# Kernel tuning notes

Measured on AMD Instinct MI355X. Metric: run time of the kernel, lower is better.

## Reference

```python
import jax, jax.numpy as jnp
import numpy as np

EPS = float(np.finfo(np.float32).eps)
B, N, NUM_ATOM, K = 16, 256, 64, 20
NUM_EDGETYPE = 3
SHORT = (1, 2, 3)
LONG = (3, 5, 7)
HIDDEN = (128, 128)
OUT = 1
SCALES = len(SHORT) + len(LONG) + NUM_EDGETYPE + 1  # 10
LB = 1e-4  # lanczos breakdown tolerance


def _xavier(k, fi, fo):
    return jax.random.uniform(k, (fi, fo), jnp.float32, -1.0, 1.0) * (6.0 / (fi + fo)) ** 0.5


def setup_inputs() -> dict:
    key = jax.random.key(0)
    ks = jax.random.split(key, 12)
    inp = {}
    inp["node_feat"] = jax.random.randint(ks[0], (B, N), 0, NUM_ATOM)
    inp["L"] = jax.random.uniform(ks[1], (B, N, N, NUM_EDGETYPE + 1), jnp.float32)
    # embedding_map: Linear(num_atom,1024) -> ReLU -> Linear(1024,num_atom)
    inp["emb_w1"] = _xavier(ks[2], NUM_ATOM, 1024); inp["emb_b1"] = jnp.zeros((1024,), jnp.float32)
    inp["emb_w2"] = _xavier(ks[3], 1024, NUM_ATOM); inp["emb_b2"] = jnp.zeros((NUM_ATOM,), jnp.float32)
    # eigen_map per long scale: Linear(K*K,1024) -> ReLU -> Linear(1024,K*K)
    S, K2 = len(LONG), K * K
    inp["eig_w1"] = jnp.stack([_xavier(jax.random.fold_in(ks[4], i), K2, 1024) for i in range(S)])
    inp["eig_b1"] = jnp.zeros((S, 1024), jnp.float32)
    inp["eig_w2"] = jnp.stack([_xavier(jax.random.fold_in(ks[5], i), 1024, K2) for i in range(S)])
    inp["eig_b2"] = jnp.zeros((S, K2), jnp.float32)
    dims = [NUM_ATOM] + list(HIDDEN) + [OUT]
    inp["filt_w0"] = _xavier(ks[6], dims[0] * SCALES, dims[1]); inp["filt_b0"] = jnp.zeros((dims[1],), jnp.float32)
    inp["filt_w1"] = _xavier(ks[7], dims[1] * SCALES, dims[2]); inp["filt_b1"] = jnp.zeros((dims[2],), jnp.float32)
    inp["filt_wo"] = _xavier(ks[8], dims[2], dims[3]); inp["filt_bo"] = jnp.zeros((dims[3],), jnp.float32)
    inp["att_w"] = _xavier(ks[9], dims[2], 1); inp["att_b"] = jnp.zeros((1,), jnp.float32)
    return inp


def _graph_laplacian(feat, adj_mask):
    # feat: B x N x D; pairwise gaussian affinity, sym-normalized (alpha=0.5)
    diff = feat[:, :, None, :] - feat[:, None, :, :]           # B,N,N,D
    dist2 = jnp.sum(diff * diff, axis=-1).reshape(B, -1)       # B,N*N
    sigma2 = jnp.mean(dist2, axis=1, keepdims=True)
    A = jnp.exp(-dist2 / sigma2).reshape(B, N, N) * adj_mask
    row_sum = jnp.sum(A, axis=2, keepdims=True)
    pad = jnp.where(row_sum == 0.0, 1.0, 0.0)
    D = 1.0 / jnp.sqrt(row_sum + pad)
    return D * A * jnp.swapaxes(D, 1, 2)


def _lanczos(A, key):
    # sequential Lanczos tridiagonalization with double Gram-Schmidt reorth
    q = jax.random.normal(key, (B, N), jnp.float32)
    q = q / jnp.linalg.norm(q, axis=1, keepdims=True)

    def step(carry, i):
        Qbuf, q_prev, qc, beta_prev, valid = carry
        z = jnp.einsum('bij,bj->bi', A, qc)
        alpha = jnp.sum(qc * z, axis=1)
        z = z - alpha[:, None] * qc - beta_prev[:, None] * q_prev
        for _ in range(2):  # reorthogonalize against Q[1..ii-1] (zero cols are no-ops)
            coef = jnp.einsum('bnk,bn->bk', Qbuf, z) / (jnp.sum(Qbuf * Qbuf, axis=1) + EPS)
            z = z - jnp.einsum('bnk,bk->bn', Qbuf, coef)
        beta = jnp.sqrt(jnp.sum(z * z, axis=1))
        valid = valid * (beta >= LB).astype(jnp.float32)
        q_next = z * valid[:, None] / (beta[:, None] + EPS)
        Qbuf = Qbuf.at[:, :, i].set(qc)
        return (Qbuf, qc, q_next, beta, valid), (alpha, beta, valid, qc)

    init = (jnp.zeros((B, N, K), jnp.float32), jnp.zeros((B, N), jnp.float32), q,
            jnp.zeros((B,), jnp.float32), jnp.ones((B,), jnp.float32))
    _, (alphas, betas, valids, qs) = jax.lax.scan(step, init, jnp.arange(K))
    alpha = alphas.T            # B,K
    beta = betas.T              # B,K
    valid = valids.T            # B,K (cumulative 1..1 0..0)
    idx = jnp.sum(valid, axis=1).astype(jnp.int32)   # rank per sample
    alpha = alpha * valid
    beta = beta[:, :K - 1] * valid[:, :K - 1]
    T = jax.vmap(lambda a, b: jnp.diag(a) + jnp.diag(b, 1) + jnp.diag(b, -1))(alpha, beta)
    Q = jnp.transpose(qs, (1, 2, 0))  # B,N,K
    # faithful to source: zero node rows >= idx_mask (only when idx < N)
    row_ok = (jnp.arange(N)[None, :] < idx[:, None]) | (idx[:, None] >= N)
    Q = Q * valid[:, None, :] * row_ok[:, :, None].astype(jnp.float32)
    return T, Q


def _spectral_filters(T, Q, eig_w1, eig_b1, eig_w2, eig_b2, key):
    T_list = []
    TT = T
    b = jax.random.normal(key, (B, K, 1), jnp.float32)
    Tb = b / jnp.linalg.norm(b, axis=1, keepdims=True)
    for ii in range(max(LONG) + 1):
        if ii in LONG:
            T_list.append(TT)
        TT = TT @ T
        # power-iteration cap on spectral radius
        Tb_new = T @ Tb
        l_max = jnp.sum(Tb_new * Tb, axis=1, keepdims=True) / (jnp.sum(Tb * Tb, axis=1, keepdims=True) + EPS)
        TT = TT * (jnp.abs(l_max) <= 1.0).astype(jnp.float32)
        Tb = Tb_new / (jnp.linalg.norm(Tb_new, axis=1, keepdims=True) + EPS)
    triu = jnp.triu(jnp.ones((K, K), jnp.float32))
    eye = jnp.eye(K, dtype=jnp.float32)
    outs = []
    for s in range(len(LONG)):
        h = jax.nn.relu(T_list[s].reshape(B, -1) @ eig_w1[s] + eig_b1[s])
        DD = (h @ eig_w2[s] + eig_b2[s]).reshape(B, K, K)
        DD = DD * triu
        DD = DD + jnp.swapaxes(DD, 1, 2) * (1.0 - eye)  # symmetrize
        outs.append(jnp.einsum('bnk,bkl,bml->bnm', Q, DD, Q))
    return jnp.stack(outs, axis=3)  # B,N,N,S


def reference(node_feat, L, emb_w1, emb_b1, emb_w2, emb_b2, eig_w1, eig_b1, eig_w2, eig_b2,
              filt_w0, filt_b0, filt_w1, filt_b1, filt_wo, filt_bo, att_w, att_b):
    key = jax.random.key(42)
    state = jax.nn.one_hot(node_feat, NUM_ATOM, dtype=jnp.float32)  # frozen identity embedding
    feat = jax.nn.relu(state @ emb_w1 + emb_b1) @ emb_w2 + emb_b2
    Lk = _graph_laplacian(feat, L[:, :, :, 0])
    T, Q = _lanczos(Lk, jax.random.fold_in(key, 0))
    filt_w = (filt_w0, filt_w1)
    filt_b = (filt_b0, filt_b1)
    for tt in range(len(HIDDEN)):
        msg = []
        DD = _spectral_filters(T, Q, eig_w1, eig_b1, eig_w2, eig_b2, jax.random.fold_in(key, tt + 1))
        tmp = state
        for ii in range(1, max(SHORT) + 1):  # short diffusion
            tmp = jnp.einsum('bij,bjd->bid', Lk, tmp)
            if ii in SHORT:
                msg.append(tmp)
        for s in range(len(LONG)):           # long (spectral) diffusion
            msg.append(jnp.einsum('bij,bjd->bid', DD[:, :, :, s], state))
        for e in range(NUM_EDGETYPE + 1):     # per-edgetype propagation
            msg.append(jnp.einsum('bij,bjd->bid', L[:, :, :, e], state))
        msg = jnp.concatenate(msg, axis=2)    # B,N,10*D
        state = jax.nn.relu(msg @ filt_w[tt] + filt_b[tt])
    y = state @ filt_wo + filt_bo             # B,N,1
    att = jax.nn.sigmoid(state @ att_w + att_b)
    score = jnp.mean(att * y, axis=1)          # B,OUT (mask=None -> mean over nodes)
    return score
```

## Files before the change

### kernel.cpp

```cpp
#include <hip/hip_runtime.h>


constexpr int nB = 16;
constexpr int nN = 256;
constexpr int nK = 20;
constexpr int QS = nN + 1;
constexpr float EPSF = 1.1920928955078125e-07f;
constexpr float LBF  = 1e-4f;

#define DEV static __device__ __forceinline__

DEV void tf2x32(unsigned k0, unsigned k1, unsigned x0, unsigned x1,
                unsigned &o0, unsigned &o1) {
  unsigned ks2 = k0 ^ k1 ^ 0x1BD11BDAu;
#define RND(r) { x0 += x1; x1 = (x1 << r) | (x1 >> (32 - r)); x1 ^= x0; }
  x0 += k0;  x1 += k1;
  RND(13) RND(15) RND(26) RND(6)
  x0 += k1;  x1 += ks2 + 1u;
  RND(17) RND(29) RND(16) RND(24)
  x0 += ks2; x1 += k0 + 2u;
  RND(13) RND(15) RND(26) RND(6)
  x0 += k0;  x1 += k1 + 3u;
  RND(17) RND(29) RND(16) RND(24)
  x0 += k1;  x1 += ks2 + 4u;
  RND(13) RND(15) RND(26) RND(6)
  x0 += ks2; x1 += k0 + 5u;
#undef RND
  o0 = x0; o1 = x1;
}

DEV float erfinv_f32(float x) {
  float w = -log1pf(-x * x);
  float p;
  if (w < 5.0f) {
    w -= 2.5f;
    p = 2.81022636e-08f;
    p = fmaf(p, w, 3.43273939e-07f);
    p = fmaf(p, w, -3.5233877e-06f);
    p = fmaf(p, w, -4.39150654e-06f);
    p = fmaf(p, w, 0.00021858087f);
    p = fmaf(p, w, -0.00125372503f);
    p = fmaf(p, w, -0.00417768164f);
    p = fmaf(p, w, 0.246640727f);
    p = fmaf(p, w, 1.50140941f);
  } else {
    w = sqrtf(w) - 3.0f;
    p = -0.000200214257f;
    p = fmaf(p, w, 0.000100950558f);
    p = fmaf(p, w, 0.00134934322f);
    p = fmaf(p, w, -0.00367342844f);
    p = fmaf(p, w, 0.00573950773f);
    p = fmaf(p, w, -0.0076224613f);
    p = fmaf(p, w, 0.00943887047f);
    p = fmaf(p, w, 1.00167406f);
    p = fmaf(p, w, 2.83297682f);
  }
  return p * x;
}

DEV float jax_normal(unsigned k0, unsigned k1, unsigned idx) {
  unsigned o0, o1;
  tf2x32(k0, k1, 0u , idx , o0, o1);
  unsigned bits = o0 ^ o1;
  float u = __uint_as_float((bits >> 9) | 0x3f800000u) - 1.0f;
  const float lo = -0.99999994f;
  float v = fmaxf(lo, u * 2.0f + lo);
  return 1.41421356237309515f * erfinv_f32(v);
}

DEV double waveRedD(double v) {
#pragma unroll
  for (int m = 32; m > 0; m >>= 1) v += __shfl_xor(v, m, 64);
  return v;
}
DEV float waveRedF(float v) {
#pragma unroll
  for (int m = 32; m > 0; m >>= 1) v += __shfl_xor(v, m, 64);
  return v;
}
DEV double blockSumD(double v, double *s4) {
  v = waveRedD(v);
  int w = threadIdx.x >> 6;
  __syncthreads();
  if ((threadIdx.x & 63) == 0) s4[w] = v;
  __syncthreads();
  return s4[0] + s4[1] + s4[2] + s4[3];
}
DEV double sum8(const double *r) {
  return ((r[0] + r[1]) + (r[2] + r[3])) + ((r[4] + r[5]) + (r[6] + r[7]));
}

__global__ __launch_bounds__(256) void feat_table_kernel(
    const float *__restrict__ w1, const float *__restrict__ b1,
    const float *__restrict__ w2, const float *__restrict__ b2,
    float *__restrict__ table) {
  int a = blockIdx.x, t = threadIdx.x;
  __shared__ float hh[1024];
  __shared__ float part[256];
  for (int k = t; k < 1024; k += 256)
    hh[k] = fmaxf(w1[(size_t)a * 1024 + k] + b1[k], 0.f);
  __syncthreads();
  int d = t & 63, slice = t >> 6;
  float acc = 0.f;
  for (int k = slice * 256; k < slice * 256 + 256; k++)
    acc += hh[k] * w2[(size_t)k * 64 + d];
  part[t] = acc;
  __syncthreads();
  if (t < 64)
    table[(size_t)a * 64 + t] =
        part[t] + part[64 + t] + part[128 + t] + part[192 + t] + b2[t];
}

__global__ __launch_bounds__(256) void feat_state_tr_kernel(
    const int *__restrict__ nf, const float *__restrict__ table,
    float *__restrict__ feat, float *__restrict__ featT,
    float *__restrict__ state0) {
  int g = blockIdx.x;
  int bb = g >> 2, n0 = (g & 3) * 64;
  int t = threadIdx.x;
  int c = t & 63, r4 = t >> 6;
  __shared__ float tl[64][65];
  __shared__ int av[64];
  if (t < 64) av[t] = nf[bb * nN + n0 + t];
  __syncthreads();
  for (int r = r4; r < 64; r += 4) {
    int a = av[r];
    float v = table[(size_t)a * 64 + c];
    tl[r][c] = v;
    feat[((size_t)(bb * nN + n0 + r)) * 64 + c] = v;
    state0[((size_t)(bb * nN + n0 + r)) * 64 + c] = (c == a) ? 1.f : 0.f;
  }
  __syncthreads();
  for (int r = r4; r < 64; r += 4)
    featT[(size_t)bb * 16384 + (size_t)r * nN + n0 + c] = tl[c][r];
}

__global__ __launch_bounds__(256) void dist2_kernel(
    const float *__restrict__ feat, const float *__restrict__ featT,
    float *__restrict__ G, double *__restrict__ part) {
  int g = blockIdx.x;
  int bb = g >> 6, i0 = (g & 63) * 4;
  int t = threadIdx.x;
  __shared__ float fi[4][64];
  __shared__ double s4[4];
  {
// ... 201 lines not shown
      Qb[i * QS + t] = qc[t];
      if (t == 0) qn2[i] = (float)sum8(redB);
    }
    __syncthreads();
    if (gid < i) {
      double p = 0.0;
#pragma unroll
      for (int j = 0; j < 16; j++) {
        int n0 = gl + 16 * j;
        p += (double)Qb[gid * QS + n0] * (double)zz[n0];
      }
#pragma unroll
      for (int m = 1; m <= 8; m <<= 1) p += __shfl_xor(p, m, 64);
      if (gl == 0)
        coef[gid] = (float)(p / ((double)qn2[gid] + (double)EPSF));
    }
    __syncthreads();
    if (h == 0) {
      double sub = 0.0;
      for (int k = 0; k < i; k++)
        sub += (double)Qb[k * QS + t] * (double)coef[k];
      zz[t] = (float)((double)zz[t] - sub);
    }
    __syncthreads();
    if (gid < i) {
      double p = 0.0;
#pragma unroll
      for (int j = 0; j < 16; j++) {
        int n0 = gl + 16 * j;
        p += (double)Qb[gid * QS + n0] * (double)zz[n0];
      }
#pragma unroll
      for (int m = 1; m <= 8; m <<= 1) p += __shfl_xor(p, m, 64);
      if (gl == 0)
        coef[gid] = (float)(p / ((double)qn2[gid] + (double)EPSF));
    }
    __syncthreads();
    double bpart = 0.0;
    if (h == 0) {
      double sub = 0.0;
      for (int k = 0; k < i; k++)
        sub += (double)Qb[k * QS + t] * (double)coef[k];
      float znew = (float)((double)zz[t] - sub);
      zz[t] = znew;
      bpart = (double)znew * (double)znew;
    }
    bpart = waveRedD(bpart);
    if (lane == 0) redA[wv] = bpart;
    __syncthreads();
    float beta = sqrtf((float)sum8(redA));
    validf *= (beta >= LBF) ? 1.f : 0.f;
    if (u == 0) {
      sAl[i] = alpha;
      sBe[i] = beta;
      sVa[i] = validf;
    }
    if (h == 0) {
      float qnext = zz[t] * validf / (beta + EPSF);
      qp[t] = qc[t];
      qc[t] = qnext;
    }
    __syncthreads();
    beta_prev = beta;
  }

  float idxf = 0.f;
  for (int k = 0; k < nK; k++) idxf += sVa[k];
  int idx = (int)idxf;
  if (h == 0) {
    float rowok = ((t < idx) || (idx >= nN)) ? 1.f : 0.f;
    for (int k = 0; k < nK; k++)
      Qout[((size_t)bb * nN + t) * nK + k] = Qb[k * QS + t] * sVa[k] * rowok;
  }
  for (int e = u; e < nK * nK; e += 512) {
    int i = e / nK, j = e % nK;
    float v = 0.f;
    if (i == j) v = sAl[i] * sVa[i];
    else if (j == i + 1) v = sBe[i] * sVa[i];
    else if (i == j + 1) v = sBe[j] * sVa[j];
    Tout[(size_t)bb * nK * nK + e] = v;
  }
}

DEV void spect_body(const float *__restrict__ Tin, float *__restrict__ Tpow2,
                    int bb, int tt, int t, char *smem) {
  float *T_  = (float *)smem;
  float *TT  = T_ + nK * nK;
  float *TTn = TT + nK * nK;
  float *Tb  = TTn + nK * nK;
  float *Tbn = Tb + nK;
  for (int e = t; e < nK * nK; e += 64) {
    float v = Tin[(size_t)bb * nK * nK + e];
    T_[e] = v;
    TT[e] = v;
  }
  unsigned k0, k1;
  tf2x32(0u, 42u, 0u, (unsigned)(tt + 1), k0, k1);
  if (t < nK) Tb[t] = jax_normal(k0, k1, (unsigned)(bb * nK + t));
  __syncthreads();
  float pv = (t < nK) ? Tb[t] * Tb[t] : 0.f;
  float nb = sqrtf(waveRedF(pv));
  if (t < nK) Tb[t] = Tb[t] / nb;
  __syncthreads();
  for (int ii = 0; ii < 8; ii++) {
    if (ii == 3 || ii == 5 || ii == 7) {
      int s = (ii - 3) / 2;
      int sf = tt * 3 + s;
      for (int e = t; e < nK * nK; e += 64)
        Tpow2[((size_t)sf * nB + bb) * nK * nK + e] = TT[e];
    }
    __syncthreads();
    for (int e = t; e < nK * nK; e += 64) {
      int i = e / nK, j = e % nK;
      float a = 0.f;
      for (int l = 0; l < nK; l++) a += TT[i * nK + l] * T_[l * nK + j];
      TTn[e] = a;
    }
    if (t < nK) {
      float a = 0.f;
      for (int l = 0; l < nK; l++) a += T_[t * nK + l] * Tb[l];
      Tbn[t] = a;
    }
    __syncthreads();
    float pn = (t < nK) ? Tbn[t] * Tb[t] : 0.f;
    float pd = (t < nK) ? Tb[t] * Tb[t] : 0.f;
    float num = waveRedF(pn);
    float den = waveRedF(pd);
    float lmax = num / (den + EPSF);
    float keep = (fabsf(lmax) <= 1.0f) ? 1.f : 0.f;
    __syncthreads();
    for (int e = t; e < nK * nK; e += 64) TT[e] = TTn[e] * keep;
    float p2 = (t < nK) ? Tbn[t] * Tbn[t] : 0.f;
    float nn = sqrtf(waveRedF(p2));
    if (t < nK) Tb[t] = Tbn[t] / (nn + EPSF);
    __syncthreads();
  }
}

DEV void eig1_body(const float *__restrict__ Tpow2, const float *__restrict__ w1p,
                   const float *__restrict__ b1p, float *__restrict__ h2,
                   int g, int t, char *smem) {
  int oc = g & 15, sf = g >> 4;
  int sw = sf % 3;
  int o = (t & 63) + oc * 64, bbg = t >> 6;
  float *tp = (float *)smem;
  for (int e = t; e < nB * 400; e += 256)
    tp[e] = Tpow2[(size_t)sf * nB * 400 + e];
  __syncthreads();
  float bias = b1p[(size_t)sw * 1024 + o];
  float acc0 = bias, acc1 = bias, acc2 = bias, acc3 = bias;
  const float *W = w1p + (size_t)sw * 400 * 1024 + o;
  const float *t0 = tp + (bbg + 0) * 400;
  const float *t1 = tp + (bbg + 4) * 400;
  const float *t2 = tp + (bbg + 8) * 400;
  const float *t3 = tp + (bbg + 12) * 400;
  for (int k = 0; k < 400; k++) {
    float w = W[(size_t)k * 1024];
    acc0 += t0[k] * w;
    acc1 += t1[k] * w;
    acc2 += t2[k] * w;
    acc3 += t3[k] * w;
  }
  h2[((size_t)sf * nB + (bbg + 0))  * 1024 + o] = fmaxf(acc0, 0.f);
  h2[((size_t)sf * nB + (bbg + 4))  * 1024 + o] = fmaxf(acc1, 0.f);
  h2[((size_t)sf * nB + (bbg + 8))  * 1024 + o] = fmaxf(acc2, 0.f);
  h2[((size_t)sf * nB + (bbg + 12)) * 1024 + o] = fmaxf(acc3, 0.f);
}

DEV void eig2_body(const float *__restrict__ h2, const float *__restrict__ w2p,
                   const float *__restrict__ b2p, float *__restrict__ raw2,
                   int g, int t, char *smem) {
  int kc = g % 25, sf = g / 25;
  int sw = sf % 3;
  int kl = (t & 15) + kc * 16, bb = t >> 4;
  float *hh = (float *)smem;
  for (int e = t; e < nB * 1024; e += 256)
    hh[(e >> 10) * 1025 + (e & 1023)] = h2[(size_t)sf * nB * 1024 + e];
  __syncthreads();
  float acc = b2p[(size_t)sw * 400 + kl];
  const float *W = w2p + (size_t)sw * 1024 * 400 + kl;
  const float *hv = hh + bb * 1025;
  for (int o = 0; o < 1024; o++) acc += hv[o] * W[(size_t)o * 400];
  raw2[((size_t)sf * nB + bb) * 400 + kl] = acc;
}

DEV void qtstate_body(const float *__restrict__ Q, const float *__restrict__ state,
                      float *__restrict__ E, int g, int t, int Din, char *smem) {
  int k = g % nK, bb = g / nK;
  float *qcol = (float *)smem;
  for (int n = t; n < nN; n += Din)
    qcol[n] = Q[((size_t)bb * nN + n) * nK + k];
  __syncthreads();
  const float *st = state + (size_t)bb * nN * Din;
  float acc = 0.f;
  for (int n = 0; n < nN; n++) acc += qcol[n] * st[(size_t)n * Din + t];
  E[((size_t)bb * nK + k) * Din + t] = acc;
}

DEV void lk_body(const float *__restrict__ Lk, const float *__restrict__ in,
                 int inStride, float *__restrict__ out, int outStride,
                 int g, int t, int Din, char *smem) {
  int bb = g >> 5, r0 = (g & 31) * 8;
  float (*rows)[nN] = (float (*)[nN])smem;
  for (int e = t; e < 8 * nN; e += Din) {
    int r = e >> 8, j = e & 255;
    rows[r][j] = Lk[((size_t)bb * nN + r0 + r) * nN + j];
  }
  __syncthreads();
  float acc[8] = {0.f, 0.f, 0.f, 0.f, 0.f, 0.f, 0.f, 0.f};
  const float *ip = in + (size_t)bb * nN * inStride + t;
  for (int j = 0; j < nN; j++) {
    float x = ip[(size_t)j * inStride];
#pragma unroll
    for (int r = 0; r < 8; r++) acc[r] += rows[r][j] * x;
  }
#pragma unroll
  for (int r = 0; r < 8; r++)
    out[((size_t)bb * nN + r0 + r) * outStride + t] = acc[r];
}

DEV void edgemsg_body(const float *__restrict__ Lfull,
                      const float *__restrict__ state, float *__restrict__ msg,
                      int C, int g, int t, int Din, char *smem) {
  int bb = g >> 6, r0 = (g & 63) * 4;
  float4 (*rows4)[nN] = (float4 (*)[nN])smem;
  const float4 *L4 = (const float4 *)Lfull;
  for (int e = t; e < 4 * nN; e += Din) {
    int r = e >> 8, j = e & 255;
    rows4[r][j] = L4[((size_t)bb * nN + r0 + r) * nN + j];
  }
  __syncthreads();
  float acc[4][4];
#pragma unroll
  for (int r = 0; r < 4; r++)
#pragma unroll
    for (int e = 0; e < 4; e++) acc[r][e] = 0.f;
  const float *st = state + (size_t)bb * nN * Din + t;
  for (int j = 0; j < nN; j++) {
    float x = st[(size_t)j * Din];
#pragma unroll
    for (int r = 0; r < 4; r++) {
      float4 lv = rows4[r][j];
      acc[r][0] += lv.x * x;
      acc[r][1] += lv.y * x;
      acc[r][2] += lv.z * x;
      acc[r][3] += lv.w * x;
    }
  }
#pragma unroll
  for (int r = 0; r < 4; r++)
#pragma unroll
    for (int e = 0; e < 4; e++)
      msg[((size_t)bb * nN + r0 + r) * C + (6 + e) * Din + t] = acc[r][e];
}

DEV void ddE_body(const float *__restrict__ raw, const float *__restrict__ E,
                  float *__restrict__ F, int g, int t, int Din, char *smem) {
  int k = g % nK, bb = (g / nK) % nB, s = g / (nK * nB);
  float *dr = (float *)smem;
  if (t < nK) {
    int mi = k < t ? k : t, ma = k < t ? t : k;
    dr[t] = raw[((size_t)s * nB + bb) * 400 + mi * nK + ma];
  }
  __syncthreads();
  float acc = 0.f;
  for (int l = 0; l < nK; l++)
    acc += dr[l] * E[((size_t)bb * nK + l) * Din + t];
  F[(((size_t)s * nB + bb) * nK + k) * Din + t] = acc;
}

DEV void longmsg_body(const float *__restrict__ Q, const float *__restrict__ F,
                      float *__restrict__ msg, int C, int g, int t, int Din,
                      char *smem) {
  int i = g % nN, bb = g / nN;
  float *qr = (float *)smem;
  if (t < nK) qr[t] = Q[((size_t)bb * nN + i) * nK + t];
  __syncthreads();
  for (int s = 0; s < 3; s++) {
    float acc = 0.f;
    for (int k = 0; k < nK; k++)
      acc += qr[k] * F[(((size_t)s * nB + bb) * nK + k) * Din + t];
    msg[((size_t)bb * nN + i) * C + (3 + s) * Din + t] = acc;
  }
}

__global__ __launch_bounds__(64) void l1d1_spect_kernel(
    const float *__restrict__ T, float *__restrict__ Tpow2) {
  __shared__ __align__(16) char smem[5120];
  int bb = blockIdx.x & 15, tt = blockIdx.x >> 4;
  spect_body(T, Tpow2, bb, tt, threadIdx.x, smem);
}

__global__ __launch_bounds__(256) void l1d2_kernel(
    const float *__restrict__ Tpow2, const float *__restrict__ w1p,
    const float *__restrict__ b1p, float *__restrict__ h2,
    const float *__restrict__ Q, const float *__restrict__ state0,
    float *__restrict__ E, const float *__restrict__ Lk,
    float *__restrict__ msg, int C) {
  __shared__ __align__(16) char smem[26240];
  int t = threadIdx.x;
  int gb = blockIdx.x;
  if (gb < 96) {
    eig1_body(Tpow2, w1p, b1p, h2, gb, t, smem);
  } else if (gb < 96 + 320) {
    int g = gb - 96;
    int k = g % nK, bb = g / nK;
    float *qcol = (float *)smem;
    for (int n = t; n < nN; n += 256)
      qcol[n] = Q[((size_t)bb * nN + n) * nK + k];
    __syncthreads();
    if (t < 64) {
      const float *st = state0 + (size_t)bb * nN * 64;
      float acc = 0.f;
      for (int n = 0; n < nN; n++) acc += qcol[n] * st[(size_t)n * 64 + t];
      E[((size_t)bb * nK + k) * 64 + t] = acc;
    }
  } else {
    int g = gb - 416;
    int bb = g >> 5, r0 = (g & 31) * 8;
    float (*rows)[nN] = (float (*)[nN])smem;
    for (int e = t; e < 8 * nN; e += 256) {
      int r = e >> 8, j = e & 255;
      rows[r][j] = Lk[((size_t)bb * nN + r0 + r) * nN + j];
    }
    __syncthreads();
    if (t < 64) {
      float acc[8] = {0.f, 0.f, 0.f, 0.f, 0.f, 0.f, 0.f, 0.f};
      const float *ip = msg + (size_t)bb * nN * C + 0 * 64 + t;
      for (int j = 0; j < nN; j++) {
        float x = ip[(size_t)j * C];
#pragma unroll
        for (int r = 0; r < 8; r++) acc[r] += rows[r][j] * x;
      }
#pragma unroll
      for (int r = 0; r < 8; r++)
        msg[((size_t)bb * nN + r0 + r) * C + 1 * 64 + t] = acc[r];
    }
  }
}

__global__ __launch_bounds__(256) void l1d3_kernel(
    const float *__restrict__ h2, const float *__restrict__ w2p,
    const float *__restrict__ b2p, float *__restrict__ raw2,
    const float *__restrict__ Lk, float *__restrict__ msg, int C) {
  __shared__ __align__(16) char smem[65600];
  int t = threadIdx.x;
  int gb = blockIdx.x;
  if (gb < 150) {
    eig2_body(h2, w2p, b2p, raw2, gb, t, smem);
  } else {
    int g = gb - 150;
    int bb = g >> 5, r0 = (g & 31) * 8;
    float (*rows)[nN] = (float (*)[nN])smem;
    for (int e = t; e < 8 * nN; e += 256) {
      int r = e >> 8, j = e & 255;
      rows[r][j] = Lk[((size_t)bb * nN + r0 + r) * nN + j];
    }
    __syncthreads();
    if (t < 64) {
      float acc[8] = {0.f, 0.f, 0.f, 0.f, 0.f, 0.f, 0.f, 0.f};
      const float *ip = msg + (size_t)bb * nN * C + 1 * 64 + t;
      for (int j = 0; j < nN; j++) {
        float x = ip[(size_t)j * C];
#pragma unroll
        for (int r = 0; r < 8; r++) acc[r] += rows[r][j] * x;
      }
#pragma unroll
      for (int r = 0; r < 8; r++)
        msg[((size_t)bb * nN + r0 + r) * C + 2 * 64 + t] = acc[r];
    }
  }
}

__global__ void msgD1_kernel(const float *__restrict__ Q,
                             const float *__restrict__ state,
                             float *__restrict__ E,
                             const float *__restrict__ Lk,
                             float *__restrict__ msg,
                             const float *__restrict__ Lfull, int C) {
  __shared__ __align__(16) char smem[16384];
  int t = threadIdx.x, Din = blockDim.x;
  int gb = blockIdx.x;
  if (gb < nB * nK) {
    qtstate_body(Q, state, E, gb, t, Din, smem);
  } else if (gb < nB * nK + nB * nN / 8) {
    lk_body(Lk, state, Din, msg + 0 * Din, C, gb - nB * nK, t, Din, smem);
  } else {
    edgemsg_body(Lfull, state, msg, C, gb - nB * nK - nB * nN / 8, t, Din, smem);
  }
}

__global__ void msgD2_kernel(const float *__restrict__ raw,
                             const float *__restrict__ E,
                             float *__restrict__ F,
                             const float *__restrict__ Lk,
                             float *__restrict__ msg, int C, int withLk) {
  __shared__ __align__(16) char smem[8192];
  int t = threadIdx.x, Din = blockDim.x;
  int gb = blockIdx.x;
  if (gb < 3 * nB * nK) {
    ddE_body(raw, E, F, gb, t, Din, smem);
  } else {
    lk_body(Lk, msg + 0 * Din, C, msg + 1 * Din, C, gb - 3 * nB * nK, t, Din,
            smem);
  }
}

__global__ void msgD3_kernel(const float *__restrict__ Q,
                             const float *__restrict__ F,
                             const float *__restrict__ Lk,
                             float *__restrict__ msg, int C) {
  __shared__ __align__(16) char smem[8192];
  int t = threadIdx.x, Din = blockDim.x;
  int gb = blockIdx.x;
  if (gb < nB * nN) {
    longmsg_body(Q, F, msg, C, gb, t, Din, smem);
  } else {
    lk_body(Lk, msg + 1 * Din, C, msg + 2 * Din, C, gb - nB * nN, t, Din, smem);
  }
}

__global__ __launch_bounds__(256) void filt_kernel(
    const float *__restrict__ msg, const float *__restrict__ W,
    const float *__restrict__ bias, float *__restrict__ out, int C) {
  int g = blockIdx.x;
  int base = g * 16;
  int t = threadIdx.x;
  int o = t & 127, ih = t >> 7;
  __shared__ float mt[16][64];
  __shared__ float wt[64][128];
  float acc[8];
  float bo = bias[o];
#pragma unroll
  for (int r = 0; r < 8; r++) acc[r] = bo;
  for (int c0 = 0; c0 < C; c0 += 64) {
    __syncthreads();
    for (int e = t; e < 16 * 64; e += 256) {
      int r = e >> 6, c = e & 63;
      mt[r][c] = msg[((size_t)(base + r)) * C + c0 + c];
    }
    for (int e = t; e < 64 * 128; e += 256)
      wt[e >> 7][e & 127] = W[(size_t)(c0 + (e >> 7)) * 128 + (e & 127)];
    __syncthreads();
    for (int c = 0; c < 64; c++) {
      float w = wt[c][o];
#pragma unroll
      for (int r = 0; r < 8; r++) acc[r] += mt[ih * 8 + r][c] * w;
    }
  }
#pragma unroll
  for (int r = 0; r < 8; r++)
    out[((size_t)(base + ih * 8 + r)) * 128 + o] = fmaxf(acc[r], 0.f);
}

__global__ __launch_bounds__(256) void score_kernel(
    const float *__restrict__ state, const float *__restrict__ wo,
    const float *__restrict__ bo, const float *__restrict__ aw,
    const float *__restrict__ ab, float *__restrict__ out) {
  __shared__ float sl[64 * 129];
  __shared__ double s4[4];
  int bb = blockIdx.x, t = threadIdx.x;
  float bof = bo[0], abf = ab[0];
  double dsum = 0.0;
  for (int r0 = 0; r0 < nN; r0 += 64) {
    __syncthreads();
    for (int e = t; e < 64 * 128; e += 256) {
      int r = e >> 7, o = e & 127;
      sl[r * 129 + o] = state[((size_t)bb * nN + r0 + r) * 128 + o];
    }
    __syncthreads();
    if (t < 64) {
      const float *sr = sl + t * 129;
      float sy = bof, sa = abf;
      for (int o = 0; o < 128; o++) {
        float v = sr[o];
        sy += v * wo[o];
        sa += v * aw[o];
      }
      float att = 1.f / (1.f + expf(-sa));
      dsum += (double)(att * sy);
    }
  }
  double m = blockSumD(dsum, s4);
  if (t == 0) out[bb] = (float)(m / (double)nN);
}

extern "C" void kernel_launch(void *const *d_in, const int *in_sizes, int n_in,
                              void *d_out, int out_size, void *d_ws,
                              size_t ws_size, hipStream_t stream) {
  (void)in_sizes; (void)n_in; (void)out_size;
  const int   *node_feat = (const int *)d_in[0];
  const float *Lfull     = (const float *)d_in[1];
  const float *emb_w1    = (const float *)d_in[2];
  const float *emb_b1    = (const float *)d_in[3];
  const float *emb_w2    = (const float *)d_in[4];
  const float *emb_b2    = (const float *)d_in[5];
  const float *eig_w1    = (const float *)d_in[6];
  const float *eig_b1    = (const float *)d_in[7];
  const float *eig_w2    = (const float *)d_in[8];
  const float *eig_b2    = (const float *)d_in[9];
  const float *filt_w0   = (const float *)d_in[10];
  const float *filt_b0   = (const float *)d_in[11];
  const float *filt_w1   = (const float *)d_in[12];
  const float *filt_b1   = (const float *)d_in[13];
  const float *filt_wo   = (const float *)d_in[14];
  const float *filt_bo   = (const float *)d_in[15];
  const float *att_w     = (const float *)d_in[16];
  const float *att_b     = (const float *)d_in[17];

  float *ws   = (float *)d_ws;
  float *G    = ws;
  float *msg  = G + 1048576;
  float *st0  = msg + 5242880;
  float *st1  = st0 + 262144;
  float *st2  = st1 + 524288;
  float *feat = st2 + 524288;
  float *table= feat + 262144;
  float *Q    = table + 4096;
  float *T    = Q + 81920;
  float *Tpow = T + 6400;
  float *DD   = Tpow + 19200;
  float *h    = DD + 19200;
  float *E    = h + 49152;
  float *F    = E + 40960;
  float *Dv   = F + 122880;
  double *part   = (double *)(Dv + 4096);
  float *GT    = msg + 4194304;
  float *featT = msg + 1048576;
  float *Tpow2 = feat;
  float *raw2  = feat + 38400;
  float *h2    = feat + 76800;
  const size_t needBytes = (size_t)(8220432) * 4;
  if (ws_size < needBytes) return;

  feat_table_kernel<<<64, 256, 0, stream>>>(emb_w1, emb_b1, emb_w2, emb_b2, table);
  feat_state_tr_kernel<<<nB * 4, 256, 0, stream>>>(node_feat, table, feat,
                                                   featT, st0);
  dist2_kernel<<<nB * 64, 256, 0, stream>>>(feat, featT, G, part);
  arow_kernel<<<nB * nN, 256, 0, stream>>>(Lfull, part, G, Dv);
  lkscale_tr_kernel<<<nB * 16, 256, 0, stream>>>(G, Dv, GT);
  lanczos_kernel<<<16 + 512 + 1024, 512, 0, stream>>>(GT, Q, T, st0, Lfull, G,
                                                      msg);

  const int QTB = nB * nK;
  const int LKB = nB * nN / 8;
  const int EDB = nB * nN / 4;
  const int DDB = 3 * nB * nK;
  const int LMB = nB * nN;

  {
    int Din = 64, C = 640;
    const float *rawT = raw2;
    l1d1_spect_kernel<<<nB * 2, 64, 0, stream>>>(T, Tpow2);
    l1d2_kernel<<<96 + QTB + LKB, 256, 0, stream>>>(Tpow2, eig_w1, eig_b1, h2,
                                                    Q, st0, E, G, msg, C);
    l1d3_kernel<<<150 + LKB, 256, 0, stream>>>(h2, eig_w2, eig_b2, raw2, G,
                                               msg, C);
    msgD2_kernel<<<DDB, Din, 0, stream>>>(rawT, E, F, G, msg, C, 0);
    msgD3_kernel<<<LMB, Din, 0, stream>>>(Q, F, G, msg, C);
    filt_kernel<<<nB * nN / 16, 256, 0, stream>>>(msg, filt_w0, filt_b0, st1, C);
  }
  {
    int Din = 128, C = 1280;
    const float *rawT = raw2 + (size_t)3 * nB * 400;
    msgD1_kernel<<<QTB + LKB + EDB, Din, 0, stream>>>(Q, st1, E, G, msg,
                                                      Lfull, C);
    msgD2_kernel<<<DDB + LKB, Din, 0, stream>>>(rawT, E, F, G, msg, C, 1);
    msgD3_kernel<<<LMB + LKB, Din, 0, stream>>>(Q, F, G, msg, C);
    filt_kernel<<<nB * nN / 16, 256, 0, stream>>>(msg, filt_w1, filt_b1, st2, C);
  }
  score_kernel<<<nB, 256, 0, stream>>>(st2, filt_wo, filt_bo, att_w, att_b,
                                       (float *)d_out);
}
```

Baseline: 602.5 us.

## Fuse post-Lanczos stages into persistent megakernel with global atomic barriers

```diff
diff --git a/kernel.cpp b/kernel.cpp
--- a/kernel.cpp
+++ b/kernel.cpp
@@ -60,7 +60,7 @@
 
 DEV float jax_normal(unsigned k0, unsigned k1, unsigned idx) {
   unsigned o0, o1;
-  tf2x32(k0, k1, 0u , idx , o0, o1);
+  tf2x32(k0, k1, 0u, idx, o0, o1);
   unsigned bits = o0 ^ o1;
   float u = __uint_as_float((bits >> 9) | 0x3f800000u) - 1.0f;
   const float lo = -0.99999994f;
@@ -428,35 +428,49 @@
   }
 }
 
-DEV void spect_body(const float *__restrict__ Tin, float *__restrict__ Tpow2,
-                    int bb, int tt, int t, char *smem) {
-  float *T_  = (float *)smem;
-  float *TT  = T_ + nK * nK;
-  float *TTn = TT + nK * nK;
-  float *Tb  = TTn + nK * nK;
+DEV void gbar(unsigned *ctr, int idx, unsigned expect) {
+  __syncthreads();
+  if (threadIdx.x == 0) {
+    __threadfence();
+    atomicAdd(&ctr[idx], 1u);
+    while (atomicAdd(&ctr[idx], 0u) < expect) __builtin_amdgcn_s_sleep(2);
+    __threadfence();
+  }
+  __syncthreads();
+}
+
+DEV void spect256(const float *Tin, float *Tpow2, int bb, int tt, int t,
+                  char *smemc, float *sKeep) {
+  float *T_  = (float *)smemc;
+  float *TT  = T_ + 400;
+  float *TTn = TT + 400;
+  float *Tb  = TTn + 400;
   float *Tbn = Tb + nK;
-  for (int e = t; e < nK * nK; e += 64) {
-    float v = Tin[(size_t)bb * nK * nK + e];
+  for (int e = t; e < 400; e += 256) {
+    float v = Tin[(size_t)bb * 400 + e];
     T_[e] = v;
     TT[e] = v;
   }
-  unsigned k0, k1;
-  tf2x32(0u, 42u, 0u, (unsigned)(tt + 1), k0, k1);
-  if (t < nK) Tb[t] = jax_normal(k0, k1, (unsigned)(bb * nK + t));
-  __syncthreads();
-  float pv = (t < nK) ? Tb[t] * Tb[t] : 0.f;
-  float nb = sqrtf(waveRedF(pv));
-  if (t < nK) Tb[t] = Tb[t] / nb;
+  if (t < nK) {
+    unsigned k0, k1;
+    tf2x32(0u, 42u, 0u, (unsigned)(tt + 1), k0, k1);
+    Tb[t] = jax_normal(k0, k1, (unsigned)(bb * nK + t));
+  }
+  __syncthreads();
+  if (t < 64) {
+    float pv = (t < nK) ? Tb[t] * Tb[t] : 0.f;
+    float nb = sqrtf(waveRedF(pv));
+    if (t < nK) Tb[t] = Tb[t] / nb;
+  }
   __syncthreads();
   for (int ii = 0; ii < 8; ii++) {
     if (ii == 3 || ii == 5 || ii == 7) {
-      int s = (ii - 3) / 2;
-      int sf = tt * 3 + s;
-      for (int e = t; e < nK * nK; e += 64)
-        Tpow2[((size_t)sf * nB + bb) * nK * nK + e] = TT[e];
-    }
-    __syncthreads();
-    for (int e = t; e < nK * nK; e += 64) {
+      int sf = tt * 3 + (ii - 3) / 2;
+      for (int e = t; e < 400; e += 256)
+        Tpow2[((size_t)sf * nB + bb) * 400 + e] = TT[e];
+    }
+    __syncthreads();
+    for (int e = t; e < 400; e += 256) {
       int i = e / nK, j = e % nK;
       float a = 0.f;
       for (int l = 0; l < nK; l++) a += TT[i * nK + l] * T_[l * nK + j];
@@ -468,28 +482,33 @@
       Tbn[t] = a;
     }
     __syncthreads();
-    float pn = (t < nK) ? Tbn[t] * Tb[t] : 0.f;
-    float pd = (t < nK) ? Tb[t] * Tb[t] : 0.f;
-    float num = waveRedF(pn);
-    float den = waveRedF(pd);
-    float lmax = num / (den + EPSF);
-    float keep = (fabsf(lmax) <= 1.0f) ? 1.f : 0.f;
-    __syncthreads();
-    for (int e = t; e < nK * nK; e += 64) TT[e] = TTn[e] * keep;
-    float p2 = (t < nK) ? Tbn[t] * Tbn[t] : 0.f;
-    float nn = sqrtf(waveRedF(p2));
-    if (t < nK) Tb[t] = Tbn[t] / (nn + EPSF);
-    __syncthreads();
-  }
-}
-
-DEV void eig1_body(const float *__restrict__ Tpow2, const float *__restrict__ w1p,
-                   const float *__restrict__ b1p, float *__restrict__ h2,
-                   int g, int t, char *smem) {
+    if (t < 64) {
+      float pn = (t < nK) ? Tbn[t] * Tb[t] : 0.f;
+      float pd = (t < nK) ? Tb[t] * Tb[t] : 0.f;
+      float num = waveRedF(pn);
+      float den = waveRedF(pd);
+      float lmax = num / (den + EPSF);
+      if (t == 0) *sKeep = (fabsf(lmax) <= 1.0f) ? 1.f : 0.f;
+    }
+    __syncthreads();
+    float keep = *sKeep;
+    for (int e = t; e < 400; e += 256) TT[e] = TTn[e] * keep;
+    if (t < 64) {
+      float p2 = (t < nK) ? Tbn[t] * Tbn[t] : 0.f;
+      float nn = sqrtf(waveRedF(p2));
+      if (t < nK) Tb[t] = Tbn[t] / (nn + EPSF);
+    }
+    __syncthreads();
+  }
+  __syncthreads();
+}
+
+DEV void eig1_256(const float *Tpow2, const float *w1p, const float *b1p,
+                  float *h2, int g, int t, char *smemc) {
   int oc = g & 15, sf = g >> 4;
   int sw = sf % 3;
   int o = (t & 63) + oc * 64, bbg = t >> 6;
-  float *tp = (float *)smem;
+  float *tp = (float *)smemc;
   for (int e = t; e < nB * 400; e += 256)
     tp[e] = Tpow2[(size_t)sf * nB * 400 + e];
   __syncthreads();
@@ -511,15 +530,15 @@
   h2[((size_t)sf * nB + (bbg + 4))  * 1024 + o] = fmaxf(acc1, 0.f);
   h2[((size_t)sf * nB + (bbg + 8))  * 1024 + o] = fmaxf(acc2, 0.f);
   h2[((size_t)sf * nB + (bbg + 12)) * 1024 + o] = fmaxf(acc3, 0.f);
-}
-
-DEV void eig2_body(const float *__restrict__ h2, const float *__restrict__ w2p,
-                   const float *__restrict__ b2p, float *__restrict__ raw2,
-                   int g, int t, char *smem) {
+  __syncthreads();
+}
+
+DEV void eig2_256(const float *h2, const float *w2p, const float *b2p,
+                  float *raw2, int g, int t, char *smemc) {
   int kc = g % 25, sf = g / 25;
   int sw = sf % 3;
   int kl = (t & 15) + kc * 16, bb = t >> 4;
-  float *hh = (float *)smem;
+  float *hh = (float *)smemc;
   for (int e = t; e < nB * 1024; e += 256)
     hh[(e >> 10) * 1025 + (e & 1023)] = h2[(size_t)sf * nB * 1024 + e];
   __syncthreads();
@@ -528,253 +547,127 @@
   const float *hv = hh + bb * 1025;
   for (int o = 0; o < 1024; o++) acc += hv[o] * W[(size_t)o * 400];
   raw2[((size_t)sf * nB + bb) * 400 + kl] = acc;
-}
-
-DEV void qtstate_body(const float *__restrict__ Q, const float *__restrict__ state,
-                      float *__restrict__ E, int g, int t, int Din, char *smem) {
+  __syncthreads();
+}
+
+DEV void qt256(const float *Q, const float *state, float *E, int g, int t,
+               int Din, char *smemc) {
   int k = g % nK, bb = g / nK;
-  float *qcol = (float *)smem;
-  for (int n = t; n < nN; n += Din)
+  float *qcol = (float *)smemc;
+  for (int n = t; n < nN; n += 256)
     qcol[n] = Q[((size_t)bb * nN + n) * nK + k];
   __syncthreads();
-  const float *st = state + (size_t)bb * nN * Din;
-  float acc = 0.f;
-  for (int n = 0; n < nN; n++) acc += qcol[n] * st[(size_t)n * Din + t];
-  E[((size_t)bb * nK + k) * Din + t] = acc;
-}
-
-DEV void lk_body(const float *__restrict__ Lk, const float *__restrict__ in,
-                 int inStride, float *__restrict__ out, int outStride,
-                 int g, int t, int Din, char *smem) {
+  if (t < Din) {
+    const float *st = state + (size_t)bb * nN * Din;
+    float acc = 0.f;
+    for (int n = 0; n < nN; n++) acc += qcol[n] * st[(size_t)n * Din + t];
+    E[((size_t)bb * nK + k) * Din + t] = acc;
+  }
+  __syncthreads();
+}
+
+DEV void lk256(const float *Lk, const float *in, int inStride, float *out,
+               int outStride, int g, int t, int Din, char *smemc) {
   int bb = g >> 5, r0 = (g & 31) * 8;
-  float (*rows)[nN] = (float (*)[nN])smem;
-  for (int e = t; e < 8 * nN; e += Din) {
+  float (*rows)[nN] = (float (*)[nN])smemc;
+  for (int e = t; e < 8 * nN; e += 256) {
     int r = e >> 8, j = e & 255;
     rows[r][j] = Lk[((size_t)bb * nN + r0 + r) * nN + j];
   }
   __syncthreads();
-  float acc[8] = {0.f, 0.f, 0.f, 0.f, 0.f, 0.f, 0.f, 0.f};
-  const float *ip = in + (size_t)bb * nN * inStride + t;
-  for (int j = 0; j < nN; j++) {
-    float x = ip[(size_t)j * inStride];
-#pragma unroll
-    for (int r = 0; r < 8; r++) acc[r] += rows[r][j] * x;
-  }
-#pragma unroll
-  for (int r = 0; r < 8; r++)
-    out[((size_t)bb * nN + r0 + r) * outStride + t] = acc[r];
-}
-
-DEV void edgemsg_body(const float *__restrict__ Lfull,
-                      const float *__restrict__ state, float *__restrict__ msg,
-                      int C, int g, int t, int Din, char *smem) {
+  if (t < Din) {
+    float acc[8] = {0.f, 0.f, 0.f, 0.f, 0.f, 0.f, 0.f, 0.f};
+    const float *ip = in + (size_t)bb * nN * inStride + t;
+    for (int j = 0; j < nN; j++) {
+      float x = ip[(size_t)j * inStride];
+#pragma unroll
+      for (int r = 0; r < 8; r++) acc[r] += rows[r][j] * x;
+    }
+#pragma unroll
+    for (int r = 0; r < 8; r++)
+      out[((size_t)bb * nN + r0 + r) * outStride + t] = acc[r];
+  }
+  __syncthreads();
+}
+
+DEV void edge256(const float *Lfull, const float *state, float *msg, int C,
+                 int g, int t, int Din, char *smemc) {
   int bb = g >> 6, r0 = (g & 63) * 4;
-  float4 (*rows4)[nN] = (float4 (*)[nN])smem;
+  float4 (*rows4)[nN] = (float4 (*)[nN])smemc;
   const float4 *L4 = (const float4 *)Lfull;
-  for (int e = t; e < 4 * nN; e += Din) {
+  for (int e = t; e < 4 * nN; e += 256) {
     int r = e >> 8, j = e & 255;
     rows4[r][j] = L4[((size_t)bb * nN + r0 + r) * nN + j];
   }
   __syncthreads();
-  float acc[4][4];
-#pragma unroll
-  for (int r = 0; r < 4; r++)
-#pragma unroll
-    for (int e = 0; e < 4; e++) acc[r][e] = 0.f;
-  const float *st = state + (size_t)bb * nN * Din + t;
-  for (int j = 0; j < nN; j++) {
-    float x = st[(size_t)j * Din];
-#pragma unroll
-    for (int r = 0; r < 4; r++) {
-      float4 lv = rows4[r][j];
-      acc[r][0] += lv.x * x;
-      acc[r][1] += lv.y * x;
-      acc[r][2] += lv.z * x;
-      acc[r][3] += lv.w * x;
-    }
-  }
-#pragma unroll
-  for (int r = 0; r < 4; r++)
-#pragma unroll
-    for (int e = 0; e < 4; e++)
-      msg[((size_t)bb * nN + r0 + r) * C + (6 + e) * Din + t] = acc[r][e];
-}
-
-DEV void ddE_body(const float *__restrict__ raw, const float *__restrict__ E,
-                  float *__restrict__ F, int g, int t, int Din, char *smem) {
+  if (t < Din) {
+    float acc[4][4];
+#pragma unroll
+    for (int r = 0; r < 4; r++)
+#pragma unroll
+      for (int e = 0; e < 4; e++) acc[r][e] = 0.f;
+    const float *st = state + (size_t)bb * nN * Din + t;
+    for (int j = 0; j < nN; j++) {
+      float x = st[(size_t)j * Din];
+#pragma unroll
+      for (int r = 0; r < 4; r++) {
+        float4 lv = rows4[r][j];
+        acc[r][0] += lv.x * x;
+        acc[r][1] += lv.y * x;
+        acc[r][2] += lv.z * x;
+        acc[r][3] += lv.w * x;
+      }
+    }
+#pragma unroll
+    for (int r = 0; r < 4; r++)
+#pragma unroll
+      for (int e = 0; e < 4; e++)
+        msg[((size_t)bb * nN + r0 + r) * C + (6 + e) * Din + t] = acc[r][e];
+  }
+  __syncthreads();
+}
+
+DEV void ddE256(const float *raw, const float *E, float *F, int g, int t,
+                int Din, char *smemc) {
   int k = g % nK, bb = (g / nK) % nB, s = g / (nK * nB);
-  float *dr = (float *)smem;
+  float *dr = (float *)smemc;
   if (t < nK) {
     int mi = k < t ? k : t, ma = k < t ? t : k;
     dr[t] = raw[((size_t)s * nB + bb) * 400 + mi * nK + ma];
   }
   __syncthreads();
-  float acc = 0.f;
-  for (int l = 0; l < nK; l++)
-    acc += dr[l] * E[((size_t)bb * nK + l) * Din + t];
-  F[(((size_t)s * nB + bb) * nK + k) * Din + t] = acc;
-}
-
-DEV void longmsg_body(const float *__restrict__ Q, const float *__restrict__ F,
-                      float *__restrict__ msg, int C, int g, int t, int Din,
-                      char *smem) {
+  if (t < Din) {
+    float acc = 0.f;
+    for (int l = 0; l < nK; l++)
+      acc += dr[l] * E[((size_t)bb * nK + l) * Din + t];
+    F[(((size_t)s * nB + bb) * nK + k) * Din + t] = acc;
+  }
+  __syncthreads();
+}
+
+DEV void longmsg256(const float *Q, const float *F, float *msg, int C, int g,
+                    int t, int Din, char *smemc) {
   int i = g % nN, bb = g / nN;
-  float *qr = (float *)smem;
+  float *qr = (float *)smemc;
   if (t < nK) qr[t] = Q[((size_t)bb * nN + i) * nK + t];
   __syncthreads();
-  for (int s = 0; s < 3; s++) {
-    float acc = 0.f;
-    for (int k = 0; k < nK; k++)
-      acc += qr[k] * F[(((size_t)s * nB + bb) * nK + k) * Din + t];
-    msg[((size_t)bb * nN + i) * C + (3 + s) * Din + t] = acc;
-  }
-}
-
-__global__ __launch_bounds__(64) void l1d1_spect_kernel(
-    const float *__restrict__ T, float *__restrict__ Tpow2) {
-  __shared__ __align__(16) char smem[5120];
-  int bb = blockIdx.x & 15, tt = blockIdx.x >> 4;
-  spect_body(T, Tpow2, bb, tt, threadIdx.x, smem);
-}
-
-__global__ __launch_bounds__(256) void l1d2_kernel(
-    const float *__restrict__ Tpow2, const float *__restrict__ w1p,
-    const float *__restrict__ b1p, float *__restrict__ h2,
-    const float *__restrict__ Q, const float *__restrict__ state0,
-    float *__restrict__ E, const float *__restrict__ Lk,
-    float *__restrict__ msg, int C) {
-  __shared__ __align__(16) char smem[26240];
-  int t = threadIdx.x;
-  int gb = blockIdx.x;
-  if (gb < 96) {
-    eig1_body(Tpow2, w1p, b1p, h2, gb, t, smem);
-  } else if (gb < 96 + 320) {
-    int g = gb - 96;
-    int k = g % nK, bb = g / nK;
-    float *qcol = (float *)smem;
-    for (int n = t; n < nN; n += 256)
-      qcol[n] = Q[((size_t)bb * nN + n) * nK + k];
-    __syncthreads();
-    if (t < 64) {
-      const float *st = state0 + (size_t)bb * nN * 64;
+  if (t < Din) {
+    for (int s = 0; s < 3; s++) {
       float acc = 0.f;
-      for (int n = 0; n < nN; n++) acc += qcol[n] * st[(size_t)n * 64 + t];
-      E[((size_t)bb * nK + k) * 64 + t] = acc;
-    }
-  } else {
-    int g = gb - 416;
-    int bb = g >> 5, r0 = (g & 31) * 8;
-    float (*rows)[nN] = (float (*)[nN])smem;
-    for (int e = t; e < 8 * nN; e += 256) {
-      int r = e >> 8, j = e & 255;
-      rows[r][j] = Lk[((size_t)bb * nN + r0 + r) * nN + j];
-    }
-    __syncthreads();
-    if (t < 64) {
-      float acc[8] = {0.f, 0.f, 0.f, 0.f, 0.f, 0.f, 0.f, 0.f};
-      const float *ip = msg + (size_t)bb * nN * C + 0 * 64 + t;
-      for (int j = 0; j < nN; j++) {
-        float x = ip[(size_t)j * C];
-#pragma unroll
-        for (int r = 0; r < 8; r++) acc[r] += rows[r][j] * x;
-      }
-#pragma unroll
-      for (int r = 0; r < 8; r++)
-        msg[((size_t)bb * nN + r0 + r) * C + 1 * 64 + t] = acc[r];
-    }
-  }
-}
-
-__global__ __launch_bounds__(256) void l1d3_kernel(
-    const float *__restrict__ h2, const float *__restrict__ w2p,
-    const float *__restrict__ b2p, float *__restrict__ raw2,
-    const float *__restrict__ Lk, float *__restrict__ msg, int C) {
-  __shared__ __align__(16) char smem[65600];
-  int t = threadIdx.x;
-  int gb = blockIdx.x;
-  if (gb < 150) {
-    eig2_body(h2, w2p, b2p, raw2, gb, t, smem);
-  } else {
-    int g = gb - 150;
-    int bb = g >> 5, r0 = (g & 31) * 8;
-    float (*rows)[nN] = (float (*)[nN])smem;
-    for (int e = t; e < 8 * nN; e += 256) {
-      int r = e >> 8, j = e & 255;
-      rows[r][j] = Lk[((size_t)bb * nN + r0 + r) * nN + j];
-    }
-    __syncthreads();
-    if (t < 64) {
-      float acc[8] = {0.f, 0.f, 0.f, 0.f, 0.f, 0.f, 0.f, 0.f};
-      const float *ip = msg + (size_t)bb * nN * C + 1 * 64 + t;
-      for (int j = 0; j < nN; j++) {
-        float x = ip[(size_t)j * C];
-#pragma unroll
-        for (int r = 0; r < 8; r++) acc[r] += rows[r][j] * x;
-      }
-#pragma unroll
-      for (int r = 0; r < 8; r++)
-        msg[((size_t)bb * nN + r0 + r) * C + 2 * 64 + t] = acc[r];
-    }
-  }
-}
-
-__global__ void msgD1_kernel(const float *__restrict__ Q,
-                             const float *__restrict__ state,
-                             float *__restrict__ E,
-                             const float *__restrict__ Lk,
-                             float *__restrict__ msg,
-                             const float *__restrict__ Lfull, int C) {
-  __shared__ __align__(16) char smem[16384];
-  int t = threadIdx.x, Din = blockDim.x;
-  int gb = blockIdx.x;
-  if (gb < nB * nK) {
-    qtstate_body(Q, state, E, gb, t, Din, smem);
-  } else if (gb < nB * nK + nB * nN / 8) {
-    lk_body(Lk, state, Din, msg + 0 * Din, C, gb - nB * nK, t, Din, smem);
-  } else {
-    edgemsg_body(Lfull, state, msg, C, gb - nB * nK - nB * nN / 8, t, Din, smem);
-  }
-}
-
-__global__ void msgD2_kernel(const float *__restrict__ raw,
-                             const float *__restrict__ E,
-                             float *__restrict__ F,
-                             const float *__restrict__ Lk,
-                             float *__restrict__ msg, int C, int withLk) {
-  __shared__ __align__(16) char smem[8192];
-  int t = threadIdx.x, Din = blockDim.x;
-  int gb = blockIdx.x;
-  if (gb < 3 * nB * nK) {
-    ddE_body(raw, E, F, gb, t, Din, smem);
-  } else {
-    lk_body(Lk, msg + 0 * Din, C, msg + 1 * Din, C, gb - 3 * nB * nK, t, Din,
-            smem);
-  }
-}
-
-__global__ void msgD3_kernel(const float *__restrict__ Q,
-                             const float *__restrict__ F,
-                             const float *__restrict__ Lk,
-                             float *__restrict__ msg, int C) {
-  __shared__ __align__(16) char smem[8192];
-  int t = threadIdx.x, Din = blockDim.x;
-  int gb = blockIdx.x;
-  if (gb < nB * nN) {
-    longmsg_body(Q, F, msg, C, gb, t, Din, smem);
-  } else {
-    lk_body(Lk, msg + 1 * Din, C, msg + 2 * Din, C, gb - nB * nN, t, Din, smem);
-  }
-}
-
-__global__ __launch_bounds__(256) void filt_kernel(
-    const float *__restrict__ msg, const float *__restrict__ W,
-    const float *__restrict__ bias, float *__restrict__ out, int C) {
-  int g = blockIdx.x;
+      for (int k = 0; k < nK; k++)
+        acc += qr[k] * F[(((size_t)s * nB + bb) * nK + k) * Din + t];
+      msg[((size_t)bb * nN + i) * C + (3 + s) * Din + t] = acc;
+    }
+  }
+  __syncthreads();
+}
+
+DEV void filt256(const float *msg, const float *W, const float *bias,
+                 float *out, int C, int g, int t, char *smemc) {
   int base = g * 16;
-  int t = threadIdx.x;
   int o = t & 127, ih = t >> 7;
-  __shared__ float mt[16][64];
-  __shared__ float wt[64][128];
+  float (*mt)[64] = (float (*)[64])smemc;
+  float (*wt)[128] = (float (*)[128])(smemc + 4096);
   float acc[8];
   float bo = bias[o];
 #pragma unroll
@@ -797,15 +690,13 @@
 #pragma unroll
   for (int r = 0; r < 8; r++)
     out[((size_t)(base + ih * 8 + r)) * 128 + o] = fmaxf(acc[r], 0.f);
-}
-
-__global__ __launch_bounds__(256) void score_kernel(
-    const float *__restrict__ state, const float *__restrict__ wo,
-    const float *__restrict__ bo, const float *__restrict__ aw,
-    const float *__restrict__ ab, float *__restrict__ out) {
-  __shared__ float sl[64 * 129];
-  __shared__ double s4[4];
-  int bb = blockIdx.x, t = threadIdx.x;
+  __syncthreads();
+}
+
+DEV void score256(const float *state, const float *wo, const float *bo,
+                  const float *aw, const float *ab, float *out, int bb, int t,
+                  char *smemc, double *s4) {
+  float *sl = (float *)smemc;
   float bof = bo[0], abf = ab[0];
   double dsum = 0.0;
   for (int r0 = 0; r0 < nN; r0 += 64) {
@@ -829,6 +720,75 @@
   }
   double m = blockSumD(dsum, s4);
   if (t == 0) out[bb] = (float)(m / (double)nN);
+}
+
+__global__ __launch_bounds__(256, 2) void mega_kernel(
+    const float *__restrict__ Q, const float *__restrict__ st0,
+    const float *__restrict__ G, const float *__restrict__ Lfull,
+    float *__restrict__ msg, float *__restrict__ E, float *__restrict__ F,
+    const float *__restrict__ T, float *__restrict__ Tpow2,
+    float *__restrict__ h2, float *__restrict__ raw2,
+    const float *__restrict__ eig_w1, const float *__restrict__ eig_b1,
+    const float *__restrict__ eig_w2, const float *__restrict__ eig_b2,
+    const float *__restrict__ filt_w0, const float *__restrict__ filt_b0,
+    const float *__restrict__ filt_w1, const float *__restrict__ filt_b1,
+    float *__restrict__ st1, float *__restrict__ st2,
+    const float *__restrict__ filt_wo, const float *__restrict__ filt_bo,
+    const float *__restrict__ att_w, const float *__restrict__ att_b,
+    float *__restrict__ out, unsigned *__restrict__ ctr) {
+  __shared__ __align__(16) char smem[65600];
+  __shared__ float sKeep;
+  __shared__ double s4[4];
+  int t = threadIdx.x;
+  const unsigned NG = gridDim.x;
+  const float *raw1 = raw2;
+  const float *rawL2 = raw2 + (size_t)3 * nB * 400;
+
+  for (int g = blockIdx.x; g < 32; g += NG)
+    spect256(T, Tpow2, g & 15, g >> 4, t, smem, &sKeep);
+  gbar(ctr, 0, NG);
+  for (int g = blockIdx.x; g < 928; g += NG) {
+    if (g < 96) eig1_256(Tpow2, eig_w1, eig_b1, h2, g, t, smem);
+    else if (g < 416) qt256(Q, st0, E, g - 96, t, 64, smem);
+    else lk256(G, msg + 0 * 64, 640, msg + 1 * 64, 640, g - 416, t, 64, smem);
+  }
+  gbar(ctr, 1, NG);
+  for (int g = blockIdx.x; g < 662; g += NG) {
+    if (g < 150) eig2_256(h2, eig_w2, eig_b2, raw2, g, t, smem);
+    else lk256(G, msg + 1 * 64, 640, msg + 2 * 64, 640, g - 150, t, 64, smem);
+  }
+  gbar(ctr, 2, NG);
+  for (int g = blockIdx.x; g < 960; g += NG)
+    ddE256(raw1, E, F, g, t, 64, smem);
+  gbar(ctr, 3, NG);
+  for (int g = blockIdx.x; g < 4096; g += NG)
+    longmsg256(Q, F, msg, 640, g, t, 64, smem);
+  gbar(ctr, 4, NG);
+  for (int g = blockIdx.x; g < 256; g += NG)
+    filt256(msg, filt_w0, filt_b0, st1, 640, g, t, smem);
+  gbar(ctr, 5, NG);
+
+  for (int g = blockIdx.x; g < 1856; g += NG) {
+    if (g < 320) qt256(Q, st1, E, g, t, 128, smem);
+    else if (g < 832) lk256(G, st1, 128, msg + 0 * 128, 1280, g - 320, t, 128, smem);
+    else edge256(Lfull, st1, msg, 1280, g - 832, t, 128, smem);
+  }
+  gbar(ctr, 6, NG);
+  for (int g = blockIdx.x; g < 1472; g += NG) {
+    if (g < 960) ddE256(rawL2, E, F, g, t, 128, smem);
+    else lk256(G, msg + 0 * 128, 1280, msg + 1 * 128, 1280, g - 960, t, 128, smem);
+  }
+  gbar(ctr, 7, NG);
+  for (int g = blockIdx.x; g < 4608; g += NG) {
+    if (g < 4096) longmsg256(Q, F, msg, 1280, g, t, 128, smem);
+    else lk256(G, msg + 1 * 128, 1280, msg + 2 * 128, 1280, g - 4096, t, 128, smem);
+  }
+  gbar(ctr, 8, NG);
+  for (int g = blockIdx.x; g < 256; g += NG)
+    filt256(msg, filt_w1, filt_b1, st2, 1280, g, t, smem);
+  gbar(ctr, 9, NG);
+  for (int g = blockIdx.x; g < 16; g += NG)
+    score256(st2, filt_wo, filt_bo, att_w, att_b, out, g, t, smem, s4);
 }
 
 extern "C" void kernel_launch(void *const *d_in, const int *in_sizes, int n_in,
@@ -876,8 +836,11 @@
   float *Tpow2 = feat;
   float *raw2  = feat + 38400;
   float *h2    = feat + 76800;
+  unsigned *ctr = (unsigned *)DD;
   const size_t needBytes = (size_t)(8220432) * 4;
   if (ws_size < needBytes) return;
+
+  hipMemsetAsync(ctr, 0, 64, stream);
 
   feat_table_kernel<<<64, 256, 0, stream>>>(emb_w1, emb_b1, emb_w2, emb_b2, table);
   feat_state_tr_kernel<<<nB * 4, 256, 0, stream>>>(node_feat, table, feat,
@@ -887,34 +850,10 @@
   lkscale_tr_kernel<<<nB * 16, 256, 0, stream>>>(G, Dv, GT);
   lanczos_kernel<<<16 + 512 + 1024, 512, 0, stream>>>(GT, Q, T, st0, Lfull, G,
                                                       msg);
-
-  const int QTB = nB * nK;
-  const int LKB = nB * nN / 8;
-  const int EDB = nB * nN / 4;
-  const int DDB = 3 * nB * nK;
-  const int LMB = nB * nN;
-
-  {
-    int Din = 64, C = 640;
-    const float *rawT = raw2;
-    l1d1_spect_kernel<<<nB * 2, 64, 0, stream>>>(T, Tpow2);
-    l1d2_kernel<<<96 + QTB + LKB, 256, 0, stream>>>(Tpow2, eig_w1, eig_b1, h2,
-                                                    Q, st0, E, G, msg, C);
-    l1d3_kernel<<<150 + LKB, 256, 0, stream>>>(h2, eig_w2, eig_b2, raw2, G,
-                                               msg, C);
-    msgD2_kernel<<<DDB, Din, 0, stream>>>(rawT, E, F, G, msg, C, 0);
-    msgD3_kernel<<<LMB, Din, 0, stream>>>(Q, F, G, msg, C);
-    filt_kernel<<<nB * nN / 16, 256, 0, stream>>>(msg, filt_w0, filt_b0, st1, C);
-  }
-  {
-    int Din = 128, C = 1280;
-    const float *rawT = raw2 + (size_t)3 * nB * 400;
-    msgD1_kernel<<<QTB + LKB + EDB, Din, 0, stream>>>(Q, st1, E, G, msg,
-                                                      Lfull, C);
-    msgD2_kernel<<<DDB + LKB, Din, 0, stream>>>(rawT, E, F, G, msg, C, 1);
-    msgD3_kernel<<<LMB + LKB, Din, 0, stream>>>(Q, F, G, msg, C);
-    filt_kernel<<<nB * nN / 16, 256, 0, stream>>>(msg, filt_w1, filt_b1, st2, C);
-  }
-  score_kernel<<<nB, 256, 0, stream>>>(st2, filt_wo, filt_bo, att_w, att_b,
-                                       (float *)d_out);
-}
+  mega_kernel<<<512, 256, 0, stream>>>(
+      Q, st0, G, Lfull, msg, E, F, T, Tpow2, h2, raw2,
+      eig_w1, eig_b1, eig_w2, eig_b2,
+      filt_w0, filt_b0, filt_w1, filt_b1,
+      st1, st2, filt_wo, filt_bo, att_w, att_b,
+      (float *)d_out, ctr);
+}
```

New measurement: 1.152 ms. 91.2% more time.
